# Kernel optimization log

Hardware: AMD Instinct MI355X
Metric: run time of the kernel (lower is better)

The kernel has to match this reference:

```python
import jax, jax.numpy as jnp
import numpy as np

T = 4          # num edge types
D = 256        # embedding_size == hidden_size
N = 100_000    # nodes
E_EDGES = 320_000
VOCAB = 10_000


def setup_inputs() -> dict:
    key = jax.random.key(0)
    ks = jax.random.split(key, 12)
    s = 0.02
    input_ids = jax.random.randint(ks[0], (1, N), 0, VOCAB)
    etype = jax.random.randint(ks[1], (1, E_EDGES), 1, T + 1)  # types 1..T
    src = jax.random.randint(ks[2], (1, E_EDGES), 0, N)
    tgt = jax.random.randint(ks[3], (1, E_EDGES), 0, N)
    typed_edges = jnp.stack([etype[0], src[0], tgt[0]], axis=0)[None]  # [1,3,E]
    embed_table = jax.random.normal(ks[4], (VOCAB, D)) * s
    # 6 inner layers (3 per concat block x 2 blocks): 256 -> 256
    edge_W_inner = jax.random.normal(ks[5], (6, T, D, 2 * D)) * s
    ln_s_inner = jnp.ones((6, D)); ln_b_inner = jnp.zeros((6, D))
    dense_W_inner = jax.random.normal(ks[6], (6, D, D)) * s
    dense_b_inner = jnp.zeros((6, D))
    # 2 output layers on concat [state, hidden]: hidden_size 512 -> 256
    edge_W_out = jax.random.normal(ks[7], (2, T, 2 * D, 4 * D)) * s
    ln_s_out = jnp.ones((2, 2 * D)); ln_b_out = jnp.zeros((2, 2 * D))
    dense_W_out = jax.random.normal(ks[8], (2, D, 2 * D)) * s
    dense_b_out = jnp.zeros((2, D))
    return {
        "input_ids": input_ids, "typed_edges": typed_edges,
        "embed_table": embed_table,
        "edge_W_inner": edge_W_inner, "ln_s_inner": ln_s_inner, "ln_b_inner": ln_b_inner,
        "dense_W_inner": dense_W_inner, "dense_b_inner": dense_b_inner,
        "edge_W_out": edge_W_out, "ln_s_out": ln_s_out, "ln_b_out": ln_b_out,
        "dense_W_out": dense_W_out, "dense_b_out": dense_b_out,
    }


def layer_norm(x, s, b, eps=1e-5):
    mu = jnp.mean(x, axis=-1, keepdims=True)
    var = jnp.mean((x - mu) ** 2, axis=-1, keepdims=True)
    return (x - mu) * jax.lax.rsqrt(var + eps) * s + b


def message_passing(state, etype, src, tgt, edge_W):
    # state [N,d]; edge_W [T, d, 2d]. Gather endpoints, per-type linear, scatter-add to targets.
    es = jnp.concatenate([state[src], state[tgt]], axis=1)  # [E, 2d]
    msgs = jnp.zeros((es.shape[0], edge_W.shape[1]), state.dtype)
    for t in range(edge_W.shape[0]):  # small fixed number of edge types
        msgs = msgs + jnp.where((etype == t + 1)[:, None], es @ edge_W[t].T, 0.0)
    return jax.ops.segment_sum(msgs, tgt, num_segments=state.shape[0])


def gnn_layer(state, etype, src, tgt, eW, ls, lb, dW, db):
    m = message_passing(state, etype, src, tgt, eW)
    h = layer_norm(jax.nn.gelu(m, approximate=False), ls, lb)
    return jnp.tanh(h @ dW.T + db)


def concat_block(state, etype, src, tgt, eWi, lsi, lbi, dWi, dbi, eWo, lso, lbo, dWo, dbo):
    x = state
    for i in range(3):
        x = gnn_layer(x, etype, src, tgt, eWi[i], lsi[i], lbi[i], dWi[i], dbi[i])
    res = jnp.concatenate([state, x], axis=1)  # [N, 2d] residual concat
    return gnn_layer(res, etype, src, tgt, eWo, lso, lbo, dWo, dbo)


def reference(input_ids, typed_edges, embed_table, edge_W_inner, ln_s_inner, ln_b_inner,
              dense_W_inner, dense_b_inner, edge_W_out, ln_s_out, ln_b_out,
              dense_W_out, dense_b_out):
    ids = input_ids[0]
    te = typed_edges[0]
    etype, src, tgt = te[0], te[1], te[2]
    x = embed_table[ids]  # [N, D]
    for b in range(2):
        sl = slice(3 * b, 3 * b + 3)
        x = concat_block(x, etype, src, tgt,
                         edge_W_inner[sl], ln_s_inner[sl], ln_b_inner[sl],
                         dense_W_inner[sl], dense_b_inner[sl],
                         edge_W_out[b], ln_s_out[b], ln_b_out[b],
                         dense_W_out[b], dense_b_out[b])
    return x
```

## Files before the change

### kernel.cpp

```cpp
#include <hip/hip_runtime.h>
#include <cstdio>

#define N_NODES 100000
#define NTILES  782
#define NE      320000
#define NCH     196
#define WCO_OFF 3145728L
#define OUT_ELEMS (N_NODES * 256)

typedef unsigned short ushort_t;
typedef unsigned short u16x4 __attribute__((ext_vector_type(4)));
typedef unsigned short u16x8 __attribute__((ext_vector_type(8)));
typedef _Float16       f16;
typedef _Float16       f16x8 __attribute__((ext_vector_type(8)));
typedef float          f32x4 __attribute__((ext_vector_type(4)));
typedef float          f32x4v __attribute__((ext_vector_type(4)));

__device__ __forceinline__ float bf2f(ushort_t u) {
    return __uint_as_float(((unsigned)u) << 16);
}
__device__ __forceinline__ ushort_t f2bf(float f) {
    unsigned u = __float_as_uint(f);
    u += 0x7FFFu + ((u >> 16) & 1u);
    return (ushort_t)(u >> 16);
}
__device__ __forceinline__ ushort_t f2h(float f) {
    f16 h = (f16)f;
    return __builtin_bit_cast(ushort_t, h);
}
__device__ __forceinline__ float h2f(ushort_t u) {
    return (float)__builtin_bit_cast(f16, u);
}

__global__ __launch_bounds__(256) void detect_k(const unsigned* __restrict__ w0, int* __restrict__ flag) {
    __shared__ int lds[256];
    int t = threadIdx.x;
    int cnt = 0;
    for (int i = t; i < 2048; i += 256) {
        unsigned e = (w0[i] >> 7) & 0xFFu;
        cnt += (e >= 96u && e <= 140u) ? 1 : 0;
    }
    lds[t] = cnt; __syncthreads();
    for (int s = 128; s > 0; s >>= 1) {
        if (t < s) lds[t] += lds[t + s];
        __syncthreads();
    }
    if (t == 0) *flag = (lds[0] < 1024) ? 1 : 0;
}

__device__ __forceinline__ ushort_t load_in(const void* p, long i, bool isf32) {
    return isf32 ? f2h(((const float*)p)[i]) : f2h(bf2f(((const ushort_t*)p)[i]));
}

struct CvtArgs {
    const void* src[8];
    ushort_t*   dst[8];
    int         n[8];
};

__global__ __launch_bounds__(256) void cvt_k(CvtArgs a, const int* __restrict__ flag) {
    int ti = blockIdx.y;
    int n = a.n[ti];
    const void* s = a.src[ti];
    ushort_t* d = a.dst[ti];
    bool isf32 = (*flag != 0);
    for (int i = blockIdx.x * 256 + threadIdx.x; i < n; i += gridDim.x * 256)
        d[i] = load_in(s, i, isf32);
}

__global__ __launch_bounds__(256) void pack_w(const void* __restrict__ eWi,
                                              const void* __restrict__ eWo,
                                              ushort_t* __restrict__ WC,
                                              const int* __restrict__ flag) {
    long idx = (long)blockIdx.x * 256 + threadIdx.x;
    bool isf32 = (*flag != 0);
    const long ELI = 6L * 4 * 256 * 512;
    const long ELO = 2L * 4 * 512 * 1024;
    if (idx < ELI) {
        int j = idx & 511;
        int o = (idx >> 9) & 255;
        int t = (idx >> 17) & 3;
        long l = idx >> 19;
        WC[l * 524288 + (long)o * 2048 + t * 512 + j] = load_in(eWi, idx, isf32);
    } else if (idx < ELI + ELO) {
        long i2 = idx - ELI;
        int j = i2 & 1023;
        int o = (i2 >> 10) & 511;
        int t = (i2 >> 19) & 3;
        long b = i2 >> 21;
        int p = t >> 1, ts = t & 1;
        WC[WCO_OFF + (b * 2 + p) * 1048576L + (long)o * 2048 + ts * 1024 + j] = load_in(eWo, i2, isf32);
    }
}

__global__ __launch_bounds__(256) void embed_k(const int* __restrict__ ids,
                                               const void* __restrict__ tab,
                                               ushort_t* __restrict__ S,
                                               const int* __restrict__ flag) {
    int row = blockIdx.x * 4 + (threadIdx.x >> 6);
    int l = threadIdx.x & 63;
    if (row >= N_NODES) return;
    int id = ids[row];
    u16x4 v;
    if (*flag) {
        f32x4v fv = *(const f32x4v*)((const float*)tab + (size_t)id * 256 + l * 4);
        #pragma unroll
        for (int i = 0; i < 4; i++) v[i] = f2h(fv[i]);
    } else {
        u16x4 bv = *(const u16x4*)((const ushort_t*)tab + (size_t)id * 256 + l * 4);
        #pragma unroll
        for (int i = 0; i < 4; i++) v[i] = f2h(bf2f(bv[i]));
    }
    *(u16x4*)(S + (size_t)row * 256 + l * 4) = v;
}

__global__ __launch_bounds__(256) void emit_k(const ushort_t* __restrict__ Bst, void* __restrict__ out,
                                              const int* __restrict__ flag) {
    long i = (long)blockIdx.x * 256 + threadIdx.x;
    if (i >= OUT_ELEMS) return;
    float v = h2f(Bst[i]);
    if (*flag) ((float*)out)[i] = v;
    else       ((ushort_t*)out)[i] = f2bf(v);
}

__global__ __launch_bounds__(256) void count_k(const int* __restrict__ tgt, int* __restrict__ counts) {
    int e = blockIdx.x * 256 + threadIdx.x;
    if (e < NE) atomicAdd(&counts[tgt[e]], 1);
}

__global__ __launch_bounds__(256) void scan1_k(const int* __restrict__ counts,
                                               int* __restrict__ incl, int* __restrict__ chsums) {
    __shared__ int lds[256];
    int c = blockIdx.x, t = threadIdx.x;
    int i0 = c * 512 + 2 * t;
    int a = (i0 < N_NODES) ? counts[i0] : 0;
    int b = (i0 + 1 < N_NODES) ? counts[i0 + 1] : 0;
    int ps = a + b;
    lds[t] = ps; __syncthreads();
    int x = ps;
    for (int off = 1; off < 256; off <<= 1) {
        int y = (t >= off) ? lds[t - off] : 0;
        __syncthreads();
        x += y; lds[t] = x;
        __syncthreads();
    }
    int excl = x - ps;
    if (i0 < N_NODES) incl[i0] = excl + a;
    if (i0 + 1 < N_NODES) incl[i0 + 1] = excl + a + b;
    if (t == 255) chsums[c] = x;
}

__global__ __launch_bounds__(256) void scan2_k(const int* __restrict__ chsums, int* __restrict__ chunkoff) {
    __shared__ int lds[256];
    int t = threadIdx.x;
    int v = (t < NCH) ? chsums[t] : 0;
    lds[t] = v; __syncthreads();
    int x = v;
    for (int off = 1; off < 256; off <<= 1) {
        int y = (t >= off) ? lds[t - off] : 0;
        __syncthreads();
        x += y; lds[t] = x;
        __syncthreads();
    }
    if (t <= NCH) chunkoff[t] = x - v;
}

__global__ __launch_bounds__(256) void scan3_k(const int* __restrict__ counts, const int* __restrict__ incl,
                                               const int* __restrict__ chunkoff,
                                               int* __restrict__ offsets, int* __restrict__ cursor) {
    int c = blockIdx.x, t = threadIdx.x;
    int base = chunkoff[c];
    #pragma unroll
    for (int k = 0; k < 2; k++) {
        int i = c * 512 + 2 * t + k;
        if (i < N_NODES) {
            int off = base + incl[i] - counts[i];
            offsets[i] = off;
            cursor[i] = off;
        }
    }
    if (c == 0 && t == 0) offsets[N_NODES] = chunkoff[NCH];
}

__global__ __launch_bounds__(256) void fill_k(const int* __restrict__ et, const int* __restrict__ src,
                                              const int* __restrict__ tgt,
                                              int* __restrict__ cursor, int* __restrict__ sorted) {
    int e = blockIdx.x * 256 + threadIdx.x;
    if (e < NE) {
        int pos = atomicAdd(&cursor[tgt[e]], 1);
        sorted[pos] = ((et[e] - 1) << 28) | src[e];
    }
}

template<int DIN>
__device__ __forceinline__ void load_row(const ushort_t* __restrict__ X0, const ushort_t* __restrict__ X1,
                                         size_t r, int l, float* out) {
    if constexpr (DIN == 256) {
        u16x4 rv = *(const u16x4*)(X0 + r * 256 + l * 4);
        #pragma unroll
        for (int i = 0; i < 4; i++) out[i] = h2f(rv[i]);
    } else {
        const ushort_t* bp = (l < 32) ? (X0 + r * 256 + (size_t)l * 8)
                                      : (X1 + r * 256 + (size_t)(l - 32) * 8);
        u16x8 rv = *(const u16x8*)bp;
        #pragma unroll
        for (int i = 0; i < 8; i++) out[i] = h2f(rv[i]);
    }
}

template<int DIN>
__device__ __forceinline__ void store_blk(ushort_t* __restrict__ G, size_t base, int l,
                                          const float* A, int D, const float* xv) {
    if constexpr (DIN == 256) {
        u16x4 o1, o2;
        #pragma unroll
        for (int i = 0; i < 4; i++) { o1[i] = f2h(A[i]); o2[i] = f2h((float)D * xv[i]); }
        *(u16x4*)(G + base + l * 4) = o1;
        *(u16x4*)(G + base + DIN + l * 4) = o2;
    } else {
        u16x8 o1, o2;
        #pragma unroll
        for (int i = 0; i < 8; i++) { o1[i] = f2h(A[i]); o2[i] = f2h((float)D * xv[i]); }
        *(u16x8*)(G + base + l * 8) = o1;
        *(u16x8*)(G + base + DIN + l * 8) = o2;
    }
}

template<int DIN, int NT>
__global__ __launch_bounds__(256) void build_g(const ushort_t* __restrict__ X0, const ushort_t* __restrict__ X1,
                                               const int* __restrict__ offsets, const int* __restrict__ sorted,
                                               ushort_t* __restrict__ G, int t0, int vbase) {
    constexpr int VPL = DIN / 64;
    int vl = blockIdx.x * 4 + (threadIdx.x >> 6);
    int l = threadIdx.x & 63;
    int v = vbase + vl;
    float a0[VPL] = {}, a1[VPL] = {}, a2[VPL] = {}, a3[VPL] = {};
    int d0 = 0, d1 = 0, d2 = 0, d3 = 0;
    float xv[VPL];
    #pragma unroll
    for (int i = 0; i < VPL; i++) xv[i] = 0.f;
    if (v < N_NODES) {
        int beg = offsets[v], end = offsets[v + 1];
        for (int e = beg; e < end; ++e) {
            int pk = sorted[e];
            int t = (pk >> 28) - t0;
            if ((unsigned)t >= (unsigned)NT) continue;
            int s = pk & 0x0FFFFFFF;
            float rvf[VPL];
            load_row<DIN>(X0, X1, (size_t)s, l, rvf);
            if (t == 0) { d0++;
                #pragma unroll
                for (int i = 0; i < VPL; i++) a0[i] += rvf[i]; }
            else if (t == 1) { d1++;
                #pragma unroll
                for (int i = 0; i < VPL; i++) a1[i] += rvf[i]; }
            else if (NT > 2 && t == 2) { d2++;
                #pragma unroll
                for (int i = 0; i < VPL; i++) a2[i] += rvf[i]; }
            else { d3++;
                #pragma unroll
                for (int i = 0; i < VPL; i++) a3[i] += rvf[i]; }
        }
        load_row<DIN>(X0, X1, (size_t)v, l, xv);
    }
    size_t rowb = (size_t)vl * 2048;
    store_blk<DIN>(G, rowb + 0 * 2 * DIN, l, a0, d0, xv);
    store_blk<DIN>(G, rowb + 1 * 2 * DIN, l, a1, d1, xv);
    if constexpr (NT > 2) {
        store_blk<DIN>(G, rowb + 2 * 2 * DIN, l, a2, d2, xv);
        store_blk<DIN>(G, rowb + 3 * 2 * DIN, l, a3, d3, xv);
    }
}

template<int EPI>
__global__ __launch_bounds__(256) void gemm_bt(const ushort_t* __restrict__ A,
                                               const ushort_t* __restrict__ B,
                                               int K, int ldc,
                                               float* __restrict__ Cf, ushort_t* __restrict__ Cb,
                                               const ushort_t* __restrict__ bias, int storeM) {
    __shared__ __align__(16) ushort_t As[128 * 64];
    __shared__ __align__(16) ushort_t Bs[128 * 64];
    const int tid = threadIdx.x;
    const int w = tid >> 6, l = tid & 63;
    const int wr = w >> 1, wc = w & 1;
    const long m0 = (long)blockIdx.y * 128, n0 = (long)blockIdx.x * 128;
    const int lr = l >> 3;
    const int lc = (l & 7) * 8;
    f32x4 acc[4][4];
    #pragma unroll
    for (int s = 0; s < 4; s++)
        #pragma unroll
        for (int n = 0; n < 4; n++) acc[s][n] = (f32x4){0.f, 0.f, 0.f, 0.f};

    for (int k0 = 0; k0 < K; k0 += 64) {
        #pragma unroll
        for (int q = 0; q < 4; q++) {
            int row = w * 32 + q * 8 + lr;
            const ushort_t* g = A + (m0 + row) * (long)K + k0 + lc;
            __builtin_amdgcn_global_load_lds(
                (__attribute__((address_space(1))) unsigned int*)(g),
                (__attribute__((address_space(3))) unsigned int*)(&As[row * 64 + lc]), 16, 0, 0);
        }
        #pragma unroll
        for (int q = 0; q < 4; q++) {
            int row = w * 32 + q * 8 + lr;
            const ushort_t* g = B + (n0 + row) * (long)K + k0 + lc;
            __builtin_amdgcn_global_load_lds(
                (__attribute__((address_space(1))) unsigned int*)(g),
                (__attribute__((address_space(3))) unsigned int*)(&Bs[row * 64 + lc]), 16, 0, 0);
        }
        __syncthreads();
        #pragma unroll
        for (int kk = 0; kk < 2; kk++) {
            f16x8 af[4], bfr[4];
            #pragma unroll
            for (int s = 0; s < 4; s++)
                af[s] = *(const f16x8*)&As[(wr * 64 + s * 16 + (l & 15)) * 64 + kk * 32 + (l >> 4) * 8];
            #pragma unroll
            for (int n = 0; n < 4; n++)
                bfr[n] = *(const f16x8*)&Bs[(wc * 64 + n * 16 + (l & 15)) * 64 + kk * 32 + (l >> 4) * 8];
            #pragma unroll
            for (int s = 0; s < 4; s++)
                #pragma unroll
                for (int n = 0; n < 4; n++)
                    acc[s][n] = __builtin_amdgcn_mfma_f32_16x16x32_f16(af[s], bfr[n], acc[s][n], 0, 0, 0);
        }
        __syncthreads();
    }
    const long rb = m0 + wr * 64 + ((l >> 4) << 2);
    const long cb = n0 + wc * 64 + (l & 15);
    #pragma unroll
    for (int s = 0; s < 4; s++) {
        #pragma unroll
        for (int n = 0; n < 4; n++) {
            long c = cb + n * 16;
            #pragma unroll
            for (int j = 0; j < 4; j++) {
                long r = rb + s * 16 + j;
                float val = acc[s][n][j];
                if constexpr (EPI == 0) {
                    Cf[r * ldc + c] = val;
                } else if constexpr (EPI == 1) {
                    Cf[r * ldc + c] += val;
                } else {
                    if (r < storeM) {
                        float t = tanhf(val + h2f(bias[c]));
                        Cb[r * ldc + c] = f2h(t);
                    }
                }
            }
        }
    }
}

template<int DOUT>
__global__ __launch_bounds__(256) void gelu_ln_k(const float* __restrict__ Mf,
                                                 const ushort_t* __restrict__ ls,
                                                 const ushort_t* __restrict__ lb,
                                                 ushort_t* __restrict__ H) {
    constexpr int VPL = DOUT / 64;
    int row = blockIdx.x * 4 + (threadIdx.x >> 6);
    int l = threadIdx.x & 63;
    const float* p = Mf + (size_t)row * DOUT + l * VPL;
    float g[VPL];
    float s = 0.f, q = 0.f;
    #pragma unroll
    for (int i = 0; i < VPL; i++) {
        float x = p[i];
        float gg = 0.5f * x * (1.f + erff(x * 0.70710678118654752f));
        g[i] = gg; s += gg; q += gg * gg;
    }
    #pragma unroll
    for (int m = 1; m < 64; m <<= 1) {
        s += __shfl_xor(s, m, 64);
        q += __shfl_xor(q, m, 64);
    }
    float mean = s * (1.f / DOUT);
    float var = q * (1.f / DOUT) - mean * mean;
    var = fmaxf(var, 0.f);
    float rs = rsqrtf(var + 1e-5f);
    ushort_t* hp = H + (size_t)row * DOUT + l * VPL;
    #pragma unroll
    for (int i = 0; i < VPL; i++) {
        int col = l * VPL + i;
        hp[i] = f2h((g[i] - mean) * rs * h2f(ls[col]) + h2f(lb[col]));
    }
}

extern "C" void kernel_launch(void* const* d_in, const int* in_sizes, int n_in,
                              void* d_out, int out_size, void* d_ws, size_t ws_size,
                              hipStream_t stream) {
    const int* ids = (const int*)d_in[0];
    const int* te = (const int*)d_in[1];
    const int* et = te;
    const int* esrc = te + NE;
    const int* etgt = te + 2 * NE;
    const void* tab = d_in[2];
    const void* eWi = d_in[3];
    const void* lsi = d_in[4];
    const void* lbi = d_in[5];
    const void* dWi = d_in[6];
    const void* dbi = d_in[7];
    const void* eWo = d_in[8];
    const void* lso = d_in[9];
    const void* lbo = d_in[10];
    const void* dWo = d_in[11];
    const void* dbo = d_in[12];

    char* w = (char*)d_ws;
    auto alloc = [&](size_t bytes) -> char* {
        char* p = w; w += (bytes + 255) & ~(size_t)255; return p;
    };
    ushort_t* A    = (ushort_t*)alloc((size_t)N_NODES * 256 * 2);
    ushort_t* Bst  = (ushort_t*)alloc((size_t)N_NODES * 256 * 2);
    ushort_t* WC   = (ushort_t*)alloc(7340032UL * 2);
    ushort_t* lsiC = (ushort_t*)alloc(1536 * 2);
    ushort_t* lbiC = (ushort_t*)alloc(1536 * 2);
    ushort_t* dbiC = (ushort_t*)alloc(1536 * 2);
    ushort_t* lsoC = (ushort_t*)alloc(1024 * 2);
    ushort_t* lboC = (ushort_t*)alloc(1024 * 2);
    ushort_t* dboC = (ushort_t*)alloc(512 * 2);
    ushort_t* dWiC = (ushort_t*)alloc(393216UL * 2);
    ushort_t* dWoC = (ushort_t*)alloc(262144UL * 2);
    int* flag      = (int*)alloc(256);
    int* counts    = (int*)alloc((size_t)N_NODES * 4);
    int* incl      = (int*)alloc((size_t)N_NODES * 4);
    int* chsums    = (int*)alloc(1024);
    int* chunkoff  = (int*)alloc(1024);
    int* offsets   = (int*)alloc((size_t)(N_NODES + 8) * 4);
    int* cursor    = (int*)alloc((size_t)N_NODES * 4);
    int* sorted    = (int*)alloc((size_t)NE * 4);
    size_t fixed = (size_t)(w - (char*)d_ws);

    const size_t per_tile = 128UL * 2048 * 2 + 128UL * 512 * 4 + 128UL * 512 * 2;
    long tiles_chunk = 0;
    if (ws_size > fixed + 4096) tiles_chunk = (long)((ws_size - fixed - 4096) / per_tile);
    if (tiles_chunk > NTILES) tiles_chunk = NTILES;
    if (tiles_chunk < 1) {
        fprintf(stderr, "kernel_launch: ws too small (%zu bytes, fixed %zu + >=%zu/chunk) -- no-op\n",
                ws_size, fixed, per_tile);
        return;
    }
    ushort_t* G  = (ushort_t*)alloc((size_t)tiles_chunk * 128 * 2048 * 2);
    float*    Mf = (float*)alloc((size_t)tiles_chunk * 128 * 512 * 4);
    ushort_t* H  = (ushort_t*)alloc((size_t)tiles_chunk * 128 * 512 * 2);
    ushort_t* R  = (ushort_t*)d_out;

    detect_k<<<1, 256, 0, stream>>>((const unsigned*)tab, flag);
    CvtArgs ca;
    ca.src[0] = lsi;  ca.dst[0] = lsiC; ca.n[0] = 1536;
    ca.src[1] = lbi;  ca.dst[1] = lbiC; ca.n[1] = 1536;
    ca.src[2] = dbi;  ca.dst[2] = dbiC; ca.n[2] = 1536;
    ca.src[3] = lso;  ca.dst[3] = lsoC; ca.n[3] = 1024;
    ca.src[4] = lbo;  ca.dst[4] = lboC; ca.n[4] = 1024;
    ca.src[5] = dbo;  ca.dst[5] = dboC; ca.n[5] = 512;
    ca.src[6] = dWi;  ca.dst[6] = dWiC; ca.n[6] = 393216;
    ca.src[7] = dWo;  ca.dst[7] = dWoC; ca.n[7] = 262144;
    cvt_k<<<dim3(1536, 8), 256, 0, stream>>>(ca, flag);
    hipMemsetAsync(counts, 0, (size_t)N_NODES * 4, stream);
    pack_w<<<28672, 256, 0, stream>>>(eWi, eWo, WC, flag);
    embed_k<<<N_NODES / 4, 256, 0, stream>>>(ids, tab, A, flag);
    count_k<<<(NE + 255) / 256, 256, 0, stream>>>(etgt, counts);
    scan1_k<<<NCH, 256, 0, stream>>>(counts, incl, chsums);
    scan2_k<<<1, 256, 0, stream>>>(chsums, chunkoff);
    scan3_k<<<NCH, 256, 0, stream>>>(counts, incl, chunkoff, offsets, cursor);
    fill_k<<<(NE + 255) / 256, 256, 0, stream>>>(et, esrc, etgt, cursor, sorted);

    auto inner_layer = [&](const ushort_t* Xin, ushort_t* Xout, int lay) {
        for (long t0t = 0; t0t < NTILES; t0t += tiles_chunk) {
            long tc = NTILES - t0t; if (tc > tiles_chunk) tc = tiles_chunk;
            long rows = tc * 128, mb = t0t * 128;
            build_g<256, 4><<<rows / 4, 256, 0, stream>>>(Xin, Xin, offsets, sorted, G, 0, (int)mb);
            gemm_bt<0><<<dim3(2, tc), 256, 0, stream>>>(G, WC + (long)lay * 524288, 2048, 256,
                                                        Mf, nullptr, nullptr, 0);
            gelu_ln_k<256><<<rows / 4, 256, 0, stream>>>(Mf, lsiC + lay * 256, lbiC + lay * 256, H);
            long sM = (long)N_NODES - mb; if (sM > rows) sM = rows; if (sM < 0) sM = 0;
            gemm_bt<2><<<dim3(2, tc), 256, 0, stream>>>(H, dWiC + (long)lay * 65536, 256, 256,
                                                        nullptr, Xout + mb * 256, dbiC + lay * 256, (int)sM);
        }
    };
    auto out_layer = [&](const ushort_t* X0, const ushort_t* X1, int b, ushort_t* dest) {
        for (long t0t = 0; t0t < NTILES; t0t += tiles_chunk) {
            long tc = NTILES - t0t; if (tc > tiles_chunk) tc = tiles_chunk;
            long rows = tc * 128, mb = t0t * 128;
            build_g<512, 2><<<rows / 4, 256, 0, stream>>>(X0, X1, offsets, sorted, G, 0, (int)mb);
            gemm_bt<0><<<dim3(4, tc), 256, 0, stream>>>(G, WC + WCO_OFF + (long)(b * 2 + 0) * 1048576,
                                                        2048, 512, Mf, nullptr, nullptr, 0);
            build_g<512, 2><<<rows / 4, 256, 0, stream>>>(X0, X1, offsets, sorted, G, 2, (int)mb);
            gemm_bt<1><<<dim3(4, tc), 256, 0, stream>>>(G, WC + WCO_OFF + (long)(b * 2 + 1) * 1048576,
                                                        2048, 512, Mf, nullptr, nullptr, 0);
            gelu_ln_k<512><<<rows / 4, 256, 0, stream>>>(Mf, lsoC + b * 512, lboC + b * 512, H);
            long sM = (long)N_NODES - mb; if (sM > rows) sM = rows; if (sM < 0) sM = 0;
            gemm_bt<2><<<dim3(2, tc), 256, 0, stream>>>(H, dWoC + (long)b * 131072, 512, 256,
                                                        nullptr, dest + mb * 256, dboC + b * 256, (int)sM);
        }
    };

    inner_layer(A, Bst, 0);
    inner_layer(Bst, R, 1);
    inner_layer(R, Bst, 2);
    out_layer(A, Bst, 0, R);
    inner_layer(R, A, 3);
    inner_layer(A, Bst, 4);
    inner_layer(Bst, A, 5);
    out_layer(R, A, 1, Bst);

    emit_k<<<(OUT_ELEMS + 255) / 256, 256, 0, stream>>>(Bst, d_out, flag);
}
```

Measured before the change: 7.106 ms.

## Transform node states before aggregation instead of gathering edge features for inner layers

The inner layers now multiply the node states by the per-type weight halves first (GEMM over N nodes producing per-type src and tgt projections), then aggregate the projected rows per target node via CSR, using degree-weighted self terms. This replaces building a 2048-wide gathered feature matrix per node and a GEMM with K=2048 with a K=256 GEMM into 512 outputs per quarter, repeated four times. The weight packing is reorganised to suit this, buffers are padded to a multiple of the tile size, and the aggregated message is stored in fp16 before GELU/LayerNorm. Rounding the message to fp16 and the changed summation order may shift numerics slightly.

Result: faster. 6.816 ms (-4.1%).

```diff
diff --git a/kernel.cpp b/kernel.cpp
--- a/kernel.cpp
+++ b/kernel.cpp
@@ -2,6 +2,7 @@
 #include <cstdio>
 
 #define N_NODES 100000
+#define NPAD    100096
 #define NTILES  782
 #define NE      320000
 #define NCH     196
@@ -81,7 +82,10 @@
         int o = (idx >> 9) & 255;
         int t = (idx >> 17) & 3;
         long l = idx >> 19;
-        WC[l * 524288 + (long)o * 2048 + t * 512 + j] = load_in(eWi, idx, isf32);
+        int q = o >> 6, oo = o & 63;
+        int k = j & 255;
+        int n = ((j < 256) ? 0 : 256) + t * 64 + oo;
+        WC[l * 524288 + (long)q * 131072 + (long)n * 256 + k] = load_in(eWi, idx, isf32);
     } else if (idx < ELI + ELO) {
         long i2 = idx - ELI;
         int j = i2 & 1023;
@@ -342,15 +346,76 @@
                     Cf[r * ldc + c] = val;
                 } else if constexpr (EPI == 1) {
                     Cf[r * ldc + c] += val;
-                } else {
+                } else if constexpr (EPI == 2) {
                     if (r < storeM) {
                         float t = tanhf(val + h2f(bias[c]));
                         Cb[r * ldc + c] = f2h(t);
                     }
+                } else {
+                    Cb[r * ldc + c] = f2h(val);
                 }
             }
         }
     }
+}
+
+__global__ __launch_bounds__(256) void agg_q(const ushort_t* __restrict__ Z,
+                                             const int* __restrict__ offsets,
+                                             const int* __restrict__ sorted,
+                                             ushort_t* __restrict__ Magg, int q) {
+    int v = blockIdx.x * 4 + (threadIdx.x >> 6);
+    int l = threadIdx.x & 63;
+    if (v >= NPAD) return;
+    ushort_t* mp = Magg + (size_t)v * 256 + (q << 6) + l;
+    if (v >= N_NODES) { *mp = 0; return; }
+    float acc = 0.f;
+    int d0 = 0, d1 = 0, d2 = 0, d3 = 0;
+    int beg = offsets[v], end = offsets[v + 1];
+    for (int e = beg; e < end; ++e) {
+        int pk = sorted[e];
+        int t = pk >> 28;
+        int s = pk & 0x0FFFFFFF;
+        acc += h2f(Z[(size_t)s * 512 + (t << 6) + l]);
+        d0 += (t == 0); d1 += (t == 1); d2 += (t == 2); d3 += (t == 3);
+    }
+    const ushort_t* zs = Z + (size_t)v * 512 + 256 + l;
+    if (d0) acc += (float)d0 * h2f(zs[0]);
+    if (d1) acc += (float)d1 * h2f(zs[64]);
+    if (d2) acc += (float)d2 * h2f(zs[128]);
+    if (d3) acc += (float)d3 * h2f(zs[192]);
+    *mp = f2h(acc);
+}
+
+__global__ __launch_bounds__(256) void gelu_ln16_k(const ushort_t* __restrict__ M,
+                                                   const ushort_t* __restrict__ ls,
+                                                   const ushort_t* __restrict__ lb,
+                                                   ushort_t* __restrict__ H) {
+    int row = blockIdx.x * 4 + (threadIdx.x >> 6);
+    int l = threadIdx.x & 63;
+    u16x4 mv = *(const u16x4*)(M + (size_t)row * 256 + l * 4);
+    float g[4];
+    float s = 0.f, q = 0.f;
+    #pragma unroll
+    for (int i = 0; i < 4; i++) {
+        float x = h2f(mv[i]);
+        float gg = 0.5f * x * (1.f + erff(x * 0.70710678118654752f));
+        g[i] = gg; s += gg; q += gg * gg;
+    }
+    #pragma unroll
+    for (int m = 1; m < 64; m <<= 1) {
+        s += __shfl_xor(s, m, 64);
+        q += __shfl_xor(q, m, 64);
+    }
+    float mean = s * (1.f / 256.f);
+    float var = q * (1.f / 256.f) - mean * mean;
+    var = fmaxf(var, 0.f);
+    float rs = rsqrtf(var + 1e-5f);
+    int col = l << 2;
+    u16x4 o;
+    #pragma unroll
+    for (int i = 0; i < 4; i++)
+        o[i] = f2h((g[i] - mean) * rs * h2f(ls[col + i]) + h2f(lb[col + i]));
+    *(u16x4*)(H + (size_t)row * 256 + col) = o;
 }
 
 template<int DOUT>
@@ -411,8 +476,8 @@
     auto alloc = [&](size_t bytes) -> char* {
         char* p = w; w += (bytes + 255) & ~(size_t)255; return p;
     };
-    ushort_t* A    = (ushort_t*)alloc((size_t)N_NODES * 256 * 2);
-    ushort_t* Bst  = (ushort_t*)alloc((size_t)N_NODES * 256 * 2);
+    ushort_t* A    = (ushort_t*)alloc((size_t)NPAD * 256 * 2);
+    ushort_t* Bst  = (ushort_t*)alloc((size_t)NPAD * 256 * 2);
     ushort_t* WC   = (ushort_t*)alloc(7340032UL * 2);
     ushort_t* lsiC = (ushort_t*)alloc(1536 * 2);
     ushort_t* lbiC = (ushort_t*)alloc(1536 * 2);
@@ -430,21 +495,28 @@
     int* offsets   = (int*)alloc((size_t)(N_NODES + 8) * 4);
     int* cursor    = (int*)alloc((size_t)N_NODES * 4);
     int* sorted    = (int*)alloc((size_t)NE * 4);
+    ushort_t* Magg = (ushort_t*)alloc((size_t)NPAD * 256 * 2);
+    ushort_t* R;
+    if ((size_t)out_size >= (size_t)NPAD * 256 * 2) R = (ushort_t*)d_out;
+    else R = (ushort_t*)alloc((size_t)NPAD * 256 * 2);
     size_t fixed = (size_t)(w - (char*)d_ws);
 
-    const size_t per_tile = 128UL * 2048 * 2 + 128UL * 512 * 4 + 128UL * 512 * 2;
-    long tiles_chunk = 0;
-    if (ws_size > fixed + 4096) tiles_chunk = (long)((ws_size - fixed - 4096) / per_tile);
+    const size_t ZQ_BYTES = (size_t)NPAD * 512 * 2;
+    const size_t PER_TILE = 128UL * 2048 * 2 + 128UL * 512 * 4 + 128UL * 512 * 2;
+    size_t bigsz = (ws_size > fixed) ? (ws_size - fixed) : 0;
+    long tiles_chunk = (long)(bigsz / PER_TILE);
     if (tiles_chunk > NTILES) tiles_chunk = NTILES;
-    if (tiles_chunk < 1) {
-        fprintf(stderr, "kernel_launch: ws too small (%zu bytes, fixed %zu + >=%zu/chunk) -- no-op\n",
-                ws_size, fixed, per_tile);
+    if (bigsz < ZQ_BYTES || tiles_chunk < 1) {
+        fprintf(stderr, "kernel_launch: ws too small (%zu bytes, fixed %zu, big %zu) -- no-op\n",
+                ws_size, fixed, bigsz);
         return;
     }
-    ushort_t* G  = (ushort_t*)alloc((size_t)tiles_chunk * 128 * 2048 * 2);
-    float*    Mf = (float*)alloc((size_t)tiles_chunk * 128 * 512 * 4);
-    ushort_t* H  = (ushort_t*)alloc((size_t)tiles_chunk * 128 * 512 * 2);
-    ushort_t* R  = (ushort_t*)d_out;
+    char* big = w;
+    ushort_t* Zq   = (ushort_t*)big;
+    ushort_t* Hin  = (ushort_t*)big;
+    ushort_t* G    = (ushort_t*)big;
+    float*    Mf   = (float*)(big + (size_t)tiles_chunk * 524288);
+    ushort_t* Hc   = (ushort_t*)(big + (size_t)tiles_chunk * (524288 + 262144));
 
     detect_k<<<1, 256, 0, stream>>>((const unsigned*)tab, flag);
     CvtArgs ca;
@@ -458,6 +530,9 @@
     ca.src[7] = dWo;  ca.dst[7] = dWoC; ca.n[7] = 262144;
     cvt_k<<<dim3(1536, 8), 256, 0, stream>>>(ca, flag);
     hipMemsetAsync(counts, 0, (size_t)N_NODES * 4, stream);
+    hipMemsetAsync(A   + (size_t)N_NODES * 256, 0, (size_t)(NPAD - N_NODES) * 256 * 2, stream);
+    hipMemsetAsync(Bst + (size_t)N_NODES * 256, 0, (size_t)(NPAD - N_NODES) * 256 * 2, stream);
+    hipMemsetAsync(R   + (size_t)N_NODES * 256, 0, (size_t)(NPAD - N_NODES) * 256 * 2, stream);
     pack_w<<<28672, 256, 0, stream>>>(eWi, eWo, WC, flag);
     embed_k<<<N_NODES / 4, 256, 0, stream>>>(ids, tab, A, flag);
     count_k<<<(NE + 255) / 256, 256, 0, stream>>>(etgt, counts);
@@ -467,18 +542,17 @@
     fill_k<<<(NE + 255) / 256, 256, 0, stream>>>(et, esrc, etgt, cursor, sorted);
 
     auto inner_layer = [&](const ushort_t* Xin, ushort_t* Xout, int lay) {
-        for (long t0t = 0; t0t < NTILES; t0t += tiles_chunk) {
-            long tc = NTILES - t0t; if (tc > tiles_chunk) tc = tiles_chunk;
-            long rows = tc * 128, mb = t0t * 128;
-            build_g<256, 4><<<rows / 4, 256, 0, stream>>>(Xin, Xin, offsets, sorted, G, 0, (int)mb);
-            gemm_bt<0><<<dim3(2, tc), 256, 0, stream>>>(G, WC + (long)lay * 524288, 2048, 256,
-                                                        Mf, nullptr, nullptr, 0);
-            gelu_ln_k<256><<<rows / 4, 256, 0, stream>>>(Mf, lsiC + lay * 256, lbiC + lay * 256, H);
-            long sM = (long)N_NODES - mb; if (sM > rows) sM = rows; if (sM < 0) sM = 0;
-            gemm_bt<2><<<dim3(2, tc), 256, 0, stream>>>(H, dWiC + (long)lay * 65536, 256, 256,
-                                                        nullptr, Xout + mb * 256, dbiC + lay * 256, (int)sM);
-        }
+        for (int q = 0; q < 4; q++) {
+            gemm_bt<3><<<dim3(4, NTILES), 256, 0, stream>>>(
+                Xin, WC + (long)lay * 524288 + (long)q * 131072, 256, 512,
+                nullptr, Zq, nullptr, 0);
+            agg_q<<<NPAD / 4, 256, 0, stream>>>(Zq, offsets, sorted, Magg, q);
+        }
+        gelu_ln16_k<<<NPAD / 4, 256, 0, stream>>>(Magg, lsiC + lay * 256, lbiC + lay * 256, Hin);
+        gemm_bt<2><<<dim3(2, NTILES), 256, 0, stream>>>(Hin, dWiC + (long)lay * 65536, 256, 256,
+                                                        nullptr, Xout, dbiC + lay * 256, N_NODES);
     };
+
     auto out_layer = [&](const ushort_t* X0, const ushort_t* X1, int b, ushort_t* dest) {
         for (long t0t = 0; t0t < NTILES; t0t += tiles_chunk) {
             long tc = NTILES - t0t; if (tc > tiles_chunk) tc = tiles_chunk;
@@ -489,9 +563,9 @@
             build_g<512, 2><<<rows / 4, 256, 0, stream>>>(X0, X1, offsets, sorted, G, 2, (int)mb);
             gemm_bt<1><<<dim3(4, tc), 256, 0, stream>>>(G, WC + WCO_OFF + (long)(b * 2 + 1) * 1048576,
                                                         2048, 512, Mf, nullptr, nullptr, 0);
-            gelu_ln_k<512><<<rows / 4, 256, 0, stream>>>(Mf, lsoC + b * 512, lboC + b * 512, H);
+            gelu_ln_k<512><<<rows / 4, 256, 0, stream>>>(Mf, lsoC + b * 512, lboC + b * 512, Hc);
             long sM = (long)N_NODES - mb; if (sM > rows) sM = rows; if (sM < 0) sM = 0;
-            gemm_bt<2><<<dim3(2, tc), 256, 0, stream>>>(H, dWoC + (long)b * 131072, 512, 256,
+            gemm_bt<2><<<dim3(2, tc), 256, 0, stream>>>(Hc, dWoC + (long)b * 131072, 512, 256,
                                                         nullptr, dest + mb * 256, dboC + b * 256, (int)sM);
         }
     };
```
